# Kernel tuning notes

Hardware: AMD Instinct MI355X
Metric: run time of the kernel (lower is better)

Reference implementation:

```python
import jax, jax.numpy as jnp
import numpy as np

NUM_NODES = 200000   # graph size
E = 128              # embedding_size
B = 256              # batch of target nodes
M = 8                # num_metapaths
L = 64               # walk length (number of (n1,n2,e) triples per metapath)
NUM_EDGE_TYPE = 8
H = 8                # num_heads (hardcoded in module)


def setup_inputs() -> dict:
    key = jax.random.key(0)
    ks = jax.random.split(key, 10)
    # walks: last dim = (n1, n2, edge_type)
    n12 = jax.random.randint(ks[0], (B, M, L, 2), 0, NUM_NODES)
    ety = jax.random.randint(ks[1], (B, M, L, 1), 0, NUM_EDGE_TYPE)
    node_mp_walks = jnp.concatenate([n12, ety], axis=-1)
    node_idx = jax.random.randint(ks[2], (B,), 0, NUM_NODES)
    mp_type_idx = jnp.arange(M)
    # fc1(onehot(n)) == node_table[n] + fc1_b  (node_table = fc1.weight.T)
    node_table = jax.random.normal(ks[3], (NUM_NODES, E), dtype=jnp.float32) * 0.1
    fc1_b = jnp.zeros((E,), dtype=jnp.float32)
    edge_table = jax.random.normal(ks[4], (NUM_EDGE_TYPE, E), dtype=jnp.float32) * 0.1
    # Indexed_LinearFC_List: one (E,E) linear per metapath
    W_mp = jax.random.normal(ks[5], (M, E, E), dtype=jnp.float32) * 0.05
    b_mp = jnp.zeros((M, E), dtype=jnp.float32)
    # MultiheadAttention params (embed_dim=E, num_heads=H, eval mode -> no dropout)
    Wqkv = jax.random.normal(ks[6], (3 * E, E), dtype=jnp.float32) * 0.05
    bqkv = jnp.zeros((3 * E,), dtype=jnp.float32)
    Wo = jax.random.normal(ks[7], (E, E), dtype=jnp.float32) * 0.05
    bo = jnp.zeros((E,), dtype=jnp.float32)
    return dict(node_idx=node_idx, mp_type_idx=mp_type_idx, node_mp_walks=node_mp_walks,
                node_table=node_table, fc1_b=fc1_b, edge_table=edge_table,
                W_mp=W_mp, b_mp=b_mp, Wqkv=Wqkv, bqkv=bqkv, Wo=Wo, bo=bo)


def reference(node_idx, mp_type_idx, node_mp_walks, node_table, fc1_b, edge_table,
              W_mp, b_mp, Wqkv, bqkv, Wo, bo):
    n1 = node_mp_walks[..., 0]          # [B,M,L]
    n2 = node_mp_walks[..., 1]
    e = node_mp_walks[..., 2]
    # gather node/edge embeddings (fc1 over one-hot == table row + bias)
    n1_vec = node_table[n1] + fc1_b     # [B,M,L,E]
    n2_vec = node_table[n2] + fc1_b     # [B,M,L,E]
    edge_vec = edge_table[e]            # [B,M,L,E]
    # elementwise fuse + mean over walk steps
    mp_agg_0 = jnp.mean(n1_vec * n2_vec * edge_vec, axis=2)        # [B,M,E]
    # per-metapath indexed linear
    Wsel = W_mp[mp_type_idx]            # [M,E,E]
    bsel = b_mp[mp_type_idx]            # [M,E]
    mp_agg_1 = jnp.einsum('bme,meo->bmo', mp_agg_0, Wsel) + bsel   # [B,M,E]
    # self-attention over metapaths (torch MHA, seq-first layout: [M,B,E])
    x = jnp.transpose(mp_agg_1, (1, 0, 2))                         # [M,B,E]
    qkv = x @ Wqkv.T + bqkv                                        # [M,B,3E]
    q, k, v = jnp.split(qkv, 3, axis=-1)
    hd = E // H
    q = q.reshape(M, B, H, hd)
    k = k.reshape(M, B, H, hd)
    v = v.reshape(M, B, H, hd)
    scores = jnp.einsum('mbhd,nbhd->bhmn', q, k) / jnp.sqrt(jnp.float32(hd))
    attn = jax.nn.softmax(scores, axis=-1)                         # [B,H,M,M]
    o = jnp.einsum('bhmn,nbhd->mbhd', attn, v).reshape(M, B, E)
    attn_output = o @ Wo.T + bo                                    # [M,B,E]
    return attn_output
```

## Files before the change

kernel.cpp:

```cpp
#include <hip/hip_runtime.h>

#define B 256
#define M 8
#define L 64
#define E 128
#define H 8
#define HD 16
#define NET 8
#define E3 384

__global__ __launch_bounds__(256, 4) void k_gather(
    const int* __restrict__ walks, const float* __restrict__ node_table,
    const float* __restrict__ fc1_b, const float* __restrict__ edge_table,
    const float* __restrict__ Wqkv, const float* __restrict__ Wo,
    float* __restrict__ WqkvT, float* __restrict__ WoT,
    float* __restrict__ agg0) {
  __shared__ int    s_idx[L][3];
  __shared__ float  s_et[NET * E];
  __shared__ float4 s_red[8][32];

  int r = blockIdx.x;
  int t = threadIdx.x;
  int g = t >> 5, lane = t & 31;

  if (t < L * 3) ((int*)s_idx)[t] = walks[r * (L * 3) + t];
  #pragma unroll
  for (int i = 0; i < 4; ++i) s_et[i * 256 + t] = edge_table[i * 256 + t];

  if (t < 32) {
    int el = r * 32 + t;
    if (el < E * E3) {
      int e = el / E3, o = el - e * E3;
      WqkvT[el] = Wqkv[o * E + e];
    } else {
      int j = el - E * E3;
      int e = j >> 7, o = j & 127;
      WoT[j] = Wo[o * E + e];
    }
  }
  __syncthreads();

  const float4* nt4 = (const float4*)node_table;
  float4 fb = ((const float4*)fc1_b)[lane];
  float4 acc = make_float4(0.f, 0.f, 0.f, 0.f);
  {
    int l0 = g * 8;
    float4 a[8], c[8];
    #pragma unroll
    for (int i = 0; i < 8; ++i) {
      int n1 = s_idx[l0 + i][0];
      int n2 = s_idx[l0 + i][1];
      a[i] = nt4[n1 * 32 + lane];
      c[i] = nt4[n2 * 32 + lane];
    }
    #pragma unroll
    for (int i = 0; i < 8; ++i) {
      int et = s_idx[l0 + i][2];
      float4 ev = ((const float4*)(s_et + et * E))[lane];
      acc.x += (a[i].x + fb.x) * (c[i].x + fb.x) * ev.x;
      acc.y += (a[i].y + fb.y) * (c[i].y + fb.y) * ev.y;
      acc.z += (a[i].z + fb.z) * (c[i].z + fb.z) * ev.z;
      acc.w += (a[i].w + fb.w) * (c[i].w + fb.w) * ev.w;
    }
  }
  s_red[g][lane] = acc;
  __syncthreads();
  if (t < 32) {
    float4 s = s_red[0][t];
    #pragma unroll
    for (int gg = 1; gg < 8; ++gg) {
      float4 v = s_red[gg][t];
      s.x += v.x; s.y += v.y; s.z += v.z; s.w += v.w;
    }
    const float inv = 1.0f / (float)L;
    s.x *= inv; s.y *= inv; s.z *= inv; s.w *= inv;
    ((float4*)agg0)[r * 32 + t] = s;
  }
}

__global__ __launch_bounds__(1024) void k_attn(
    const float* __restrict__ agg0, const int* __restrict__ mp_type_idx,
    const float* __restrict__ W_mp, const float* __restrict__ b_mp,
    const float* __restrict__ WqkvT, const float* __restrict__ bqkv,
    const float* __restrict__ WoT, const float* __restrict__ bo,
    float* __restrict__ out) {
  __shared__ float s_x[M][E];
  __shared__ float s_y[M][E];
  __shared__ float s_qkv[M][E3 + 1];
  __shared__ float s_sc[H][M][M];
  __shared__ float s_o[M][E];
  __shared__ int   s_mp[M];

  int b = blockIdx.x;
  int t = threadIdx.x;

  ((float*)s_x)[t] = agg0[b * (M * E) + t];
  if (t < M) s_mp[t] = mp_type_idx[t];
  __syncthreads();

  {
    int m = t >> 7, o = t & 127;
    int mp = s_mp[m];
    const float* W = W_mp + mp * E * E;
    float acc = 0.f;
    for (int e = 0; e < E; ++e)
      acc += s_x[m][e] * W[e * E + o];
    s_y[m][o] = acc + b_mp[mp * E + o];
  }
  __syncthreads();

  if (t < 768) {
    int half = t / 384;
    int o = t - half * 384;
    float acc[4] = {0.f, 0.f, 0.f, 0.f};
    for (int e = 0; e < E; ++e) {
      float w = WqkvT[e * E3 + o];
      #pragma unroll
      for (int j = 0; j < 4; ++j) acc[j] += s_y[half * 4 + j][e] * w;
    }
    float bias = bqkv[o];
    #pragma unroll
    for (int j = 0; j < 4; ++j) s_qkv[half * 4 + j][o] = acc[j] + bias;
  }
  __syncthreads();

  if (t < 512) {
    int h = t >> 6, mq = (t >> 3) & 7, n = t & 7;
    float s = 0.f;
    #pragma unroll
    for (int d = 0; d < HD; ++d)
      s += s_qkv[mq][h * HD + d] * s_qkv[n][E + h * HD + d];
    s_sc[h][mq][n] = s * 0.25f;
  }
  __syncthreads();

  if (t < 64) {
    int h = t >> 3, mq = t & 7;
    float mx = -1e30f;
    #pragma unroll
    for (int n = 0; n < 8; ++n) mx = fmaxf(mx, s_sc[h][mq][n]);
    float ex[8];
    float sum = 0.f;
    #pragma unroll
    for (int n = 0; n < 8; ++n) { ex[n] = __expf(s_sc[h][mq][n] - mx); sum += ex[n]; }
    float inv = 1.0f / sum;
    #pragma unroll
    for (int n = 0; n < 8; ++n) s_sc[h][mq][n] = ex[n] * inv;
  }
  __syncthreads();

  {
    int mq = t >> 7, col = t & 127, h = col >> 4;
    float s = 0.f;
    #pragma unroll
    for (int n = 0; n < 8; ++n)
      s += s_sc[h][mq][n] * s_qkv[n][2 * E + col];
    s_o[mq][col] = s;
  }
  __syncthreads();

  if (t < 512) {
    int pm = t >> 7, o = t & 127;
    float acc[2] = {0.f, 0.f};
    for (int e = 0; e < E; ++e) {
      float w = WoT[e * E + o];
      acc[0] += s_o[pm * 2][e] * w;
      acc[1] += s_o[pm * 2 + 1][e] * w;
    }
    float bias = bo[o];
    out[((pm * 2) * B + b) * E + o]     = acc[0] + bias;
    out[((pm * 2 + 1) * B + b) * E + o] = acc[1] + bias;
  }
}

extern "C" void kernel_launch(void* const* d_in, const int* in_sizes, int n_in,
                              void* d_out, int out_size, void* d_ws, size_t ws_size,
                              hipStream_t stream) {
  const int*   mp_type_idx = (const int*)d_in[1];
  const int*   walks       = (const int*)d_in[2];
  const float* node_table  = (const float*)d_in[3];
  const float* fc1_b       = (const float*)d_in[4];
  const float* edge_table  = (const float*)d_in[5];
  const float* W_mp        = (const float*)d_in[6];
  const float* b_mp        = (const float*)d_in[7];
  const float* Wqkv        = (const float*)d_in[8];
  const float* bqkv        = (const float*)d_in[9];
  const float* Wo          = (const float*)d_in[10];
  const float* bo          = (const float*)d_in[11];
  float* out = (float*)d_out;

  char* ws = (char*)d_ws;
  float* WqkvT = (float*)(ws);
  float* WoT   = (float*)(ws + (192 << 10));
  float* agg0  = (float*)(ws + (256 << 10));

  k_gather<<<dim3(B * M), dim3(256), 0, stream>>>(
      walks, node_table, fc1_b, edge_table, Wqkv, Wo, WqkvT, WoT, agg0);
  k_attn<<<dim3(B), dim3(1024), 0, stream>>>(
      agg0, mp_type_idx, W_mp, b_mp, WqkvT, bqkv, WoT, bo, out);
}
```

Baseline: 193.7 us.

## Stream node-table gathers directly into LDS with double-buffered async loads

Replaces the register-based gather of node embeddings with __builtin_amdgcn_global_load_lds, which writes each 16-byte load straight into a per-wave LDS staging buffer. The work is regrouped into 4 wave64s handling 16 walk steps each, issued in two alternating chunk buffers with explicit s_waitcnt vmcnt so compute on one chunk overlaps the loads for the next. The aim is to cut register pressure and keep more random-row gathers in flight. In exchange it adds 32 KB of LDS per block, which can lower occupancy, and it relies on hand-written waitcnt counts and on the builtin's per-lane LDS layout being correct.

Result: no change. 193.7 us (-0.0%).

```diff
diff --git a/kernel.cpp b/kernel.cpp
--- a/kernel.cpp
+++ b/kernel.cpp
@@ -1,4 +1,5 @@
 #include <hip/hip_runtime.h>
+#include <stdint.h>
 
 #define B 256
 #define M 8
@@ -9,21 +10,25 @@
 #define NET 8
 #define E3 384
 
+typedef const __attribute__((address_space(1))) void* gas1_t;
+typedef __attribute__((address_space(3))) void* las3_t;
+
 __global__ __launch_bounds__(256, 4) void k_gather(
     const int* __restrict__ walks, const float* __restrict__ node_table,
     const float* __restrict__ fc1_b, const float* __restrict__ edge_table,
     const float* __restrict__ Wqkv, const float* __restrict__ Wo,
     float* __restrict__ WqkvT, float* __restrict__ WoT,
     float* __restrict__ agg0) {
-  __shared__ int    s_idx[L][3];
+  __shared__ int    s_idx[L * 3];
   __shared__ float  s_et[NET * E];
-  __shared__ float4 s_red[8][32];
+  __shared__ float  s_stage[4][2][4 * 256];
+  __shared__ float2 s_red[4][64];
 
   int r = blockIdx.x;
   int t = threadIdx.x;
-  int g = t >> 5, lane = t & 31;
-
-  if (t < L * 3) ((int*)s_idx)[t] = walks[r * (L * 3) + t];
+  int w = t >> 6, lane = t & 63;
+
+  if (t < L * 3) s_idx[t] = walks[r * (L * 3) + t];
   #pragma unroll
   for (int i = 0; i < 4; ++i) s_et[i * 256 + t] = edge_table[i * 256 + t];
 
@@ -40,41 +45,66 @@
   }
   __syncthreads();
 
-  const float4* nt4 = (const float4*)node_table;
-  float4 fb = ((const float4*)fc1_b)[lane];
-  float4 acc = make_float4(0.f, 0.f, 0.f, 0.f);
-  {
-    int l0 = g * 8;
-    float4 a[8], c[8];
-    #pragma unroll
-    for (int i = 0; i < 8; ++i) {
-      int n1 = s_idx[l0 + i][0];
-      int n2 = s_idx[l0 + i][1];
-      a[i] = nt4[n1 * 32 + lane];
-      c[i] = nt4[n2 * 32 + lane];
-    }
-    #pragma unroll
-    for (int i = 0; i < 8; ++i) {
-      int et = s_idx[l0 + i][2];
-      float4 ev = ((const float4*)(s_et + et * E))[lane];
-      acc.x += (a[i].x + fb.x) * (c[i].x + fb.x) * ev.x;
-      acc.y += (a[i].y + fb.y) * (c[i].y + fb.y) * ev.y;
-      acc.z += (a[i].z + fb.z) * (c[i].z + fb.z) * ev.z;
-      acc.w += (a[i].w + fb.w) * (c[i].w + fb.w) * ev.w;
-    }
-  }
-  s_red[g][lane] = acc;
-  __syncthreads();
-  if (t < 32) {
-    float4 s = s_red[0][t];
-    #pragma unroll
-    for (int gg = 1; gg < 8; ++gg) {
-      float4 v = s_red[gg][t];
-      s.x += v.x; s.y += v.y; s.z += v.z; s.w += v.w;
+  const float* nt = node_table;
+  int sub = lane & 31;
+  int second = lane >> 5;
+
+  float2 fb = ((const float2*)fc1_b)[lane];
+  float2 acc = make_float2(0.f, 0.f);
+
+  auto issue_chunk = [&](int c, int buf) {
+    #pragma unroll
+    for (int i = 0; i < 4; ++i) {
+      int sl = (w << 4) + (c << 2) + i;
+      int n1 = s_idx[sl * 3 + 0];
+      int n2 = s_idx[sl * 3 + 1];
+      int row = second ? n2 : n1;
+      const float* src = nt + (size_t)row * E + sub * 4;
+      __builtin_amdgcn_global_load_lds((gas1_t)src,
+                                       (las3_t)&s_stage[w][buf][i * 256],
+                                       16, 0, 0);
+    }
+  };
+  auto compute_chunk = [&](int c, int buf) {
+    #pragma unroll
+    for (int i = 0; i < 4; ++i) {
+      int sl = (w << 4) + (c << 2) + i;
+      int et = s_idx[sl * 3 + 2];
+      float2 a  = *(const float2*)&s_stage[w][buf][i * 256 + 2 * lane];
+      float2 cc = *(const float2*)&s_stage[w][buf][i * 256 + 128 + 2 * lane];
+      float2 ev = *(const float2*)&s_et[et * E + 2 * lane];
+      acc.x += (a.x + fb.x) * (cc.x + fb.x) * ev.x;
+      acc.y += (a.y + fb.y) * (cc.y + fb.y) * ev.y;
+    }
+  };
+
+  issue_chunk(0, 0);
+  issue_chunk(1, 1);
+  asm volatile("s_waitcnt vmcnt(4)" ::: "memory");
+  compute_chunk(0, 0);
+  asm volatile("" ::: "memory");
+  issue_chunk(2, 0);
+  asm volatile("s_waitcnt vmcnt(4)" ::: "memory");
+  compute_chunk(1, 1);
+  asm volatile("" ::: "memory");
+  issue_chunk(3, 1);
+  asm volatile("s_waitcnt vmcnt(4)" ::: "memory");
+  compute_chunk(2, 0);
+  asm volatile("s_waitcnt vmcnt(0)" ::: "memory");
+  compute_chunk(3, 1);
+
+  s_red[w][lane] = acc;
+  __syncthreads();
+  if (t < 64) {
+    float2 s = s_red[0][t];
+    #pragma unroll
+    for (int ww = 1; ww < 4; ++ww) {
+      float2 v = s_red[ww][t];
+      s.x += v.x; s.y += v.y;
     }
     const float inv = 1.0f / (float)L;
-    s.x *= inv; s.y *= inv; s.z *= inv; s.w *= inv;
-    ((float4*)agg0)[r * 32 + t] = s;
+    s.x *= inv; s.y *= inv;
+    ((float2*)agg0)[r * 64 + t] = s;
   }
 }
 
```
